# Kernel tuning notes

Measured on AMD Instinct MI355X. Metric: run time of the kernel, lower is better.

The kernel has to match this reference:

```python
import jax, jax.numpy as jnp
import numpy as np

LEAK = 0.01  # torch F.leaky_relu default
EPS = 1e-5   # torch LayerNorm default


def _ln(x, g, b):
    mu = jnp.mean(x, axis=-1, keepdims=True)
    var = jnp.var(x, axis=-1, keepdims=True)
    return (x - mu) * jax.lax.rsqrt(var + EPS) * g + b


def setup_inputs() -> dict:
    key = jax.random.key(0)
    ks = jax.random.split(key, 12)
    npeds, h, e = 8192, 256, 64
    s = 0.05
    return {
        "last_pos": jax.random.normal(ks[0], (npeds, 2), jnp.float32),
        "last_pos_rel": jax.random.normal(ks[1], (npeds, 2), jnp.float32),
        "h0": jax.random.normal(ks[2], (1, npeds, h), jnp.float32) * s,
        "c0": jax.random.normal(ks[3], (1, npeds, h), jnp.float32) * s,
        "W_ih": jax.random.normal(ks[4], (4 * h, e), jnp.float32) * s,
        "W_hh": jax.random.normal(ks[5], (4 * h, h), jnp.float32) * s,
        "b_ih": jax.random.normal(ks[6], (4 * h,), jnp.float32) * s,
        "b_hh": jax.random.normal(ks[7], (4 * h,), jnp.float32) * s,
        "emb_W": jax.random.normal(ks[8], (e, 2), jnp.float32) * s,
        "emb_b": jax.random.normal(ks[9], (e,), jnp.float32) * s,
        "ln1_g": jnp.ones((2,), jnp.float32),
        "ln1_b": jnp.zeros((2,), jnp.float32),
        "pos_W": jax.random.normal(ks[10], (2, h), jnp.float32) * s,
        "pos_b": jax.random.normal(ks[11], (2,), jnp.float32) * s,
        "ln2_g": jnp.ones((h,), jnp.float32),
        "ln2_b": jnp.zeros((h,), jnp.float32),
    }


def reference(last_pos, last_pos_rel, h0, c0, W_ih, W_hh, b_ih, b_hh,
              emb_W, emb_b, ln1_g, ln1_b, pos_W, pos_b, ln2_g, ln2_b):
    seq_len = 30
    h_dim = W_hh.shape[1]
    bias = b_ih + b_hh

    def embed(p):  # leaky_relu(spatial_embedding(ln1(p)))
        return jax.nn.leaky_relu(_ln(p, ln1_g, ln1_b) @ emb_W.T + emb_b, LEAK)

    def step(carry, _):
        dec_in, h, c, lp = carry  # dec_in [N,e], h/c [N,H], lp [N,2]
        gates = dec_in @ W_ih.T + h @ W_hh.T + bias  # [N,4H]
        i, f, g, o = jnp.split(gates, 4, axis=-1)    # torch gate order i,f,g,o
        c = jax.nn.sigmoid(f) * c + jax.nn.sigmoid(i) * jnp.tanh(g)
        h = jax.nn.sigmoid(o) * jnp.tanh(c)
        rel = jax.nn.sigmoid(_ln(h, ln2_g, ln2_b) @ pos_W.T + pos_b)  # [N,2]
        lp = rel + lp
        return (embed(rel), h, c, lp), rel

    carry0 = (embed(last_pos_rel), h0[0], c0[0], last_pos)
    _, rels = jax.lax.scan(step, carry0, None, length=seq_len)
    return rels  # [seq_len, npeds, 2]
```

## Files before the change

### kernel.cpp

```cpp
#include <hip/hip_runtime.h>


typedef float  f32x4  __attribute__((ext_vector_type(4)));
typedef short  short8 __attribute__((ext_vector_type(8)));
typedef __bf16 bf16x8 __attribute__((ext_vector_type(8)));
typedef int    i32x4  __attribute__((ext_vector_type(4)));

#define WS_W     0
#define WS_HBUF  (640 * 1024)
#define WS_BIAS  (WS_HBUF + 8388608)
#define WS_SCAL  (WS_BIAS + 4096)
#define WS_CTR   (WS_SCAL + 64)

__device__ __forceinline__ unsigned short f2bf(float f) {
  unsigned int u = __float_as_uint(f);
  u += 0x7FFFu + ((u >> 16) & 1u);
  return (unsigned short)(u >> 16);
}
__device__ __forceinline__ float bf2f(short s) {
  return __uint_as_float(((unsigned int)(unsigned short)s) << 16);
}
__device__ __forceinline__ float sigm(float x) {
  return __builtin_amdgcn_rcpf(1.0f + __expf(-x));
}
__device__ __forceinline__ float tanh_(float x) {
  float ax = fabsf(x);
  float t = __expf(-2.0f * ax);
  float r = (1.0f - t) * __builtin_amdgcn_rcpf(1.0f + t);
  return x >= 0.0f ? r : -r;
}
__device__ __forceinline__ f32x4 mfma16(short8 a, short8 b, f32x4 c) {
  return __builtin_amdgcn_mfma_f32_16x16x32_bf16(
      __builtin_bit_cast(bf16x8, a), __builtin_bit_cast(bf16x8, b), c, 0, 0, 0);
}
__device__ __forceinline__ void sc_store16(void* p, i32x4 v) {
  asm volatile("global_store_dwordx4 %0, %1, off sc0 sc1" ::"v"(p), "v"(v)
               : "memory");
}
__device__ __forceinline__ void drain_vm() {
  asm volatile("s_waitcnt vmcnt(0)" ::: "memory");
}
__device__ __forceinline__ void batch_load6(const i32x4* p0, const i32x4* p1,
                                            const i32x4* p2, const i32x4* p3,
                                            const i32x4* p4, const i32x4* p5,
                                            i32x4& r0, i32x4& r1, i32x4& r2,
                                            i32x4& r3, i32x4& r4, i32x4& r5) {
  asm volatile(
      "global_load_dwordx4 %0, %6, off sc0 sc1\n\t"
      "global_load_dwordx4 %1, %7, off sc0 sc1\n\t"
      "global_load_dwordx4 %2, %8, off sc0 sc1\n\t"
      "global_load_dwordx4 %3, %9, off sc0 sc1\n\t"
      "global_load_dwordx4 %4, %10, off sc0 sc1\n\t"
      "global_load_dwordx4 %5, %11, off sc0 sc1\n\t"
      "s_waitcnt vmcnt(0)"
      : "=&v"(r0), "=&v"(r1), "=&v"(r2), "=&v"(r3), "=&v"(r4), "=&v"(r5)
      : "v"(p0), "v"(p1), "v"(p2), "v"(p3), "v"(p4), "v"(p5)
      : "memory");
}

extern "C" __global__ void shuffle_weights(const float* __restrict__ Wih,
                                           const float* __restrict__ Whh,
                                           unsigned short* __restrict__ ws_w) {
  int t = blockIdx.x * 256 + threadIdx.x;
  if (t >= 40960) return;
  int l = t & 63;
  int x = t >> 6;
  int uw = x & 3;
  int g = (x >> 2) & 3;
  int y = x >> 4;
  int kc = y % 10;
  int ug = y / 10;
  int row = g * 256 + ug * 64 + uw * 16 + (l & 15);
  unsigned short* dst = ws_w + (size_t)t * 8;
  if (kc < 2) {
    const float* src = Wih + row * 64 + kc * 32 + (l >> 4) * 8;
#pragma unroll
    for (int j = 0; j < 8; j++) dst[j] = f2bf(src[j]);
  } else {
    const float* src = Whh + row * 256 + (kc - 2) * 32 + (l >> 4) * 8;
#pragma unroll
    for (int j = 0; j < 8; j++) dst[j] = f2bf(src[j]);
  }
}

extern "C" __global__ void prologue2(const float* __restrict__ b_ih,
                                     const float* __restrict__ b_hh,
                                     const float* __restrict__ ln2g,
                                     const float* __restrict__ ln2b,
                                     const float* __restrict__ posW,
                                     float* __restrict__ biasv,
                                     float* __restrict__ scal,
                                     int* __restrict__ ctr) {
  int t = threadIdx.x;
#pragma unroll
  for (int k2 = 0; k2 < 4; k2++) {
    int n = t * 4 + k2;
    biasv[n] = b_ih[n] + b_hh[n];
  }
  if (t < 64) ctr[t * 64] = 0;
  __shared__ float red[256][4];
  float g = ln2g[t], b = ln2b[t], p0 = posW[t], p1 = posW[256 + t];
  red[t][0] = b * p0;
  red[t][1] = b * p1;
  red[t][2] = g * p0;
  red[t][3] = g * p1;
  __syncthreads();
  for (int s = 128; s > 0; s >>= 1) {
    if (t < s) {
#pragma unroll
      for (int v = 0; v < 4; v++) red[t][v] += red[t + s][v];
    }
    __syncthreads();
  }
  if (t == 0) {
#pragma unroll
    for (int v = 0; v < 4; v++) scal[v] = red[0][v];
  }
}

extern "C" __global__ __launch_bounds__(512, 2) void decoder_main(
    const float* __restrict__ lpr, const float* __restrict__ h0,
    const float* __restrict__ c0, const float* __restrict__ embW,
    const float* __restrict__ embB, const float* __restrict__ ln1g,
    const float* __restrict__ ln1b, const float* __restrict__ posW,
    const float* __restrict__ posB, const float* __restrict__ ln2g,
    const unsigned short* __restrict__ ws_w,
    unsigned short* __restrict__ hbuf,
    const float* __restrict__ biasv, const float* __restrict__ scal,
    int* __restrict__ ctr, float* __restrict__ out) {
  __shared__ unsigned short w_lds[4 * 16 * 512];
  __shared__ unsigned short h_stage[8 * 8 * 512];
  __shared__ unsigned short xh[16 * 512];
  __shared__ float ppt[512];
  __shared__ float n01[128][2];

  const int bid = blockIdx.x;
  const int pg = bid >> 2, ug = bid & 3;
  const int tid = threadIdx.x;
  const int w = tid >> 6, l = tid & 63;
  const int uw = w & 3, pw = w >> 2;
  const int q = l >> 4, li = l & 15;
  const int P0 = pg * 128;
  const int loff = l * 8;
  const int u = ug * 64 + uw * 16 + li;

  {
    const unsigned short* src = ws_w + (size_t)ug * 81920;
#pragma unroll
    for (int it = 0; it < 8; it++) {
      int f = tid + it * 512;
      *(short8*)(w_lds + f * 8) = *(const short8*)(src + f * 8);
    }
  }
  short8 wr[6][4];
#pragma unroll
  for (int kk = 0; kk < 6; kk++)
#pragma unroll
    for (int g = 0; g < 4; g++)
      wr[kk][g] = *(const short8*)(ws_w + (size_t)ug * 81920 +
                                   ((kk + 4) * 16 + g * 4 + uw) * 512 + loff);

  const float K0 = scal[0], K1 = scal[1], SP0 = scal[2], SP1 = scal[3];
  const float pb0 = posB[0], pb1 = posB[1];
  const float g10 = ln1g[0], g11 = ln1g[1], b10 = ln1b[0], b11 = ln1b[1];

  float bias_r[4];
#pragma unroll
  for (int g = 0; g < 4; g++) bias_r[g] = biasv[g * 256 + u];

  {
    int uu = tid & 255, r = tid >> 8;
    ppt[uu * 2 + r] = ln2g[uu] * posW[r * 256 + uu];
  }

  f32x4 c_r[4];
#pragma unroll
  for (int mt = 0; mt < 4; mt++)
#pragma unroll
    for (int r = 0; r < 4; r++)
      c_r[mt][r] = c0[(size_t)(P0 + pw * 64 + mt * 16 + q * 4 + r) * 256 + u];

#pragma unroll
  for (int it = 0; it < 8; it++) {
    int f = tid + it * 512;
    int ll = f & 63, kc = (f >> 6) & 7, Tl = f >> 9;
    const float* src =
        h0 + (size_t)(P0 + Tl * 16 + (ll & 15)) * 256 + kc * 32 + (ll >> 4) * 8;
    float tf[8];
    *(float4*)&tf[0] = *(const float4*)(src);
    *(float4*)&tf[4] = *(const float4*)(src + 4);
    short8 sv;
#pragma unroll
    for (int j = 0; j < 8; j++) sv[j] = (short)f2bf(tf[j]);
    *(short8*)(h_stage + f * 8) = sv;
  }

  if (tid < 128) {
    float r0 = lpr[(P0 + tid) * 2], r1 = lpr[(P0 + tid) * 2 + 1];
    float d = 0.5f * (r0 - r1);
    float rs = rsqrtf(d * d + 1e-5f);
    n01[tid][0] = d * rs * g10 + b10;
    n01[tid][1] = -d * rs * g11 + b11;
  }
  __syncthreads();

  {
    const int pc = tid >> 2, s4 = tid & 3;
    float n0 = n01[pc][0], n1 = n01[pc][1];
    int Tl = pc >> 4, row = pc & 15;
#pragma unroll
    for (int jj = 0; jj < 16; jj++) {
      int k = s4 * 16 + jj;
      float e = n0 * embW[k * 2] + n1 * embW[k * 2 + 1] + embB[k];
      e = e > 0.f ? e : 0.01f * e;
      xh[(Tl * 2 + (k >> 5)) * 512 + (row + 16 * ((k & 31) >> 3)) * 8 + (k & 7)] =
          f2bf(e);
    }
  }
  __syncthreads();

  i32x4* hb4 = (i32x4*)hbuf;

  for (int st = 0; st < 30; st++) {
    const size_t pbase = (size_t)(st & 1) * 262144;

    f32x4 acc[4][4];
#pragma unroll
    for (int g = 0; g < 4; g++)
#pragma unroll
      for (int mt = 0; mt < 4; mt++)
        acc[g][mt] = (f32x4){bias_r[g], bias_r[g], bias_r[g], bias_r[g]};

#pragma unroll
    for (int kc2 = 0; kc2 < 2; kc2++) {
      short8 ax[4];
#pragma unroll
      for (int mt = 0; mt < 4; mt++)
        ax[mt] = *(const short8*)(xh + ((pw * 4 + mt) * 2 + kc2) * 512 + loff);
#pragma unroll
      for (int g = 0; g < 4; g++) {
        short8 b = *(const short8*)(w_lds + (kc2 * 16 + g * 4 + uw) * 512 + loff);
#pragma unroll
        for (int mt = 0; mt < 4; mt++)
          acc[g][mt] = mfma16(ax[mt], b, acc[g][mt]);
      }
    }
#pragma unroll
    for (int kc = 0; kc < 8; kc++) {
      short8 a[4];
#pragma unroll
      for (int mt = 0; mt < 4; mt++)
        a[mt] = *(const short8*)(h_stage + ((pw * 4 + mt) * 8 + kc) * 512 + loff);
      if (kc < 2) {
#pragma unroll
        for (int g = 0; g < 4; g++) {
          short8 b =
              *(const short8*)(w_lds + ((kc + 2) * 16 + g * 4 + uw) * 512 + loff);
#pragma unroll
          for (int mt = 0; mt < 4; mt++)
            acc[g][mt] = mfma16(a[mt], b, acc[g][mt]);
        }
      } else {
#pragma unroll
        for (int g = 0; g < 4; g++)
#pragma unroll
          for (int mt = 0; mt < 4; mt++)
            acc[g][mt] = mfma16(a[mt], wr[kc - 2][g], acc[g][mt]);
      }
    }
    __syncthreads();

#pragma unroll
    for (int mt = 0; mt < 4; mt++) {
#pragma unroll
      for (int r = 0; r < 4; r++) {
        float iv = sigm(acc[0][mt][r]);
        float fv = sigm(acc[1][mt][r]);
        float gv = tanh_(acc[2][mt][r]);
        float ov = sigm(acc[3][mt][r]);
        float cc = fv * c_r[mt][r] + iv * gv;
        c_r[mt][r] = cc;
        float hv = ov * tanh_(cc);
        xh[((pw * 4 + mt) * 2 + (uw >> 1)) * 512 +
           ((q * 4 + r) + 16 * ((uw & 1) * 2 + (li >> 3))) * 8 + (li & 7)] =
            f2bf(hv);
      }
    }
    __syncthreads();

    i32x4 vown[2];
    {
      const i32x4* xh4 = (const i32x4*)xh;
#pragma unroll
      for (int it = 0; it < 2; it++) {
        int f = tid + it * 512;
        int s = f & 63, c = f >> 6, Tl = c >> 1, kcl = c & 1;
        vown[it] = xh4[f];
        sc_store16(hb4 + pbase + (((size_t)(pg * 8 + Tl)) * 8 + 2 * ug + kcl) * 64 + s,
                   vown[it]);
      }
      drain_vm();
    }
    __syncthreads();

    if (tid == 0) {
      __hip_atomic_fetch_add(ctr + pg * 64, 1, __ATOMIC_RELAXED,
                             __HIP_MEMORY_SCOPE_AGENT);
      int target = 4 * (st + 1);
      while (__hip_atomic_load(ctr + pg * 64, __ATOMIC_RELAXED,
                               __HIP_MEMORY_SCOPE_AGENT) < target)
        __builtin_amdgcn_s_sleep(1);
    }
    __syncthreads();

    {
      const i32x4* ps[6];
      int Tls[6], kcs[6], ss[6];
#pragma unroll
      for (int it = 0; it < 6; it++) {
        int f = tid + it * 512;
        int s = f & 63, x = f >> 6;
        int Tl = x / 6, j = x - Tl * 6;
        int kc = j + (j >= 2 * ug ? 2 : 0);
        Tls[it] = Tl; kcs[it] = kc; ss[it] = s;
        ps[it] = hb4 + pbase + (((size_t)(pg * 8 + Tl)) * 8 + kc) * 64 + s;
      }
      i32x4 r0, r1, r2, r3, r4, r5;
      batch_load6(ps[0], ps[1], ps[2], ps[3], ps[4], ps[5], r0, r1, r2, r3, r4,
                  r5);
      i32x4* hs4 = (i32x4*)h_stage;
      hs4[(Tls[0] * 8 + kcs[0]) * 64 + ss[0]] = r0;
      hs4[(Tls[1] * 8 + kcs[1]) * 64 + ss[1]] = r1;
      hs4[(Tls[2] * 8 + kcs[2]) * 64 + ss[2]] = r2;
      hs4[(Tls[3] * 8 + kcs[3]) * 64 + ss[3]] = r3;
      hs4[(Tls[4] * 8 + kcs[4]) * 64 + ss[4]] = r4;
      hs4[(Tls[5] * 8 + kcs[5]) * 64 + ss[5]] = r5;
#pragma unroll
      for (int it = 0; it < 2; it++) {
        int f = tid + it * 512;
        int s = f & 63, c = f >> 6, Tl = c >> 1, kcl = c & 1;
        hs4[(Tl * 8 + 2 * ug + kcl) * 64 + s] = vown[it];
      }
    }
    __syncthreads();

    {
      const int pl = tid >> 2, part = tid & 3;
      const int Tl = pl >> 4, row = pl & 15;
      float S = 0.f, S2 = 0.f, D0 = 0.f, D1 = 0.f;
#pragma unroll
      for (int kk = 0; kk < 2; kk++) {
        int kcx = part * 2 + kk;
#pragma unroll
        for (int sub = 0; sub < 4; sub++) {
          short8 h8 = *(const short8*)(h_stage + (Tl * 8 + kcx) * 512 +
                                       (row + 16 * sub) * 8);
          const float4* pp = (const float4*)(ppt + (kcx * 32 + sub * 8) * 2);
#pragma unroll
          for (int k4 = 0; k4 < 4; k4++) {
            float4 pv = pp[k4];
            float ha = bf2f(h8[2 * k4]);
            float hb = bf2f(h8[2 * k4 + 1]);
            S += ha + hb;
            S2 += ha * ha + hb * hb;
            D0 += ha * pv.x + hb * pv.z;
            D1 += ha * pv.y + hb * pv.w;
          }
        }
      }
      S += __shfl_xor(S, 1, 64);  S += __shfl_xor(S, 2, 64);
      S2 += __shfl_xor(S2, 1, 64); S2 += __shfl_xor(S2, 2, 64);
      D0 += __shfl_xor(D0, 1, 64); D0 += __shfl_xor(D0, 2, 64);
      D1 += __shfl_xor(D1, 1, 64); D1 += __shfl_xor(D1, 2, 64);
      if (part == 0) {
        float mu = S * (1.0f / 256.0f);
        float var = S2 * (1.0f / 256.0f) - mu * mu;
        float rsig = rsqrtf(var + 1e-5f);
        float rel0 = sigm(rsig * (D0 - mu * SP0) + K0 + pb0);
        float rel1 = sigm(rsig * (D1 - mu * SP1) + K1 + pb1);
        if (ug == 0)
          *(float2*)(out + (size_t)st * 16384 + (P0 + pl) * 2) =
              make_float2(rel0, rel1);
        float d = 0.5f * (rel0 - rel1);
        float rs = rsqrtf(d * d + 1e-5f);
        n01[pl][0] = d * rs * g10 + b10;
        n01[pl][1] = -d * rs * g11 + b11;
      }
    }
    __syncthreads();

    if (st < 29) {
      const int pc = tid >> 2, s4 = tid & 3;
      float n0 = n01[pc][0], n1 = n01[pc][1];
      int Tl = pc >> 4, row = pc & 15;
#pragma unroll
      for (int jj = 0; jj < 16; jj++) {
        int k = s4 * 16 + jj;
        float e = n0 * embW[k * 2] + n1 * embW[k * 2 + 1] + embB[k];
        e = e > 0.f ? e : 0.01f * e;
        xh[(Tl * 2 + (k >> 5)) * 512 + (row + 16 * ((k & 31) >> 3)) * 8 +
           (k & 7)] = f2bf(e);
      }
    }
    __syncthreads();
  }
}

extern "C" void kernel_launch(void* const* d_in, const int* in_sizes, int n_in,
                              void* d_out, int out_size, void* d_ws,
                              size_t ws_size, hipStream_t stream) {
  (void)in_sizes; (void)n_in; (void)out_size; (void)ws_size;
  const float* lpr  = (const float*)d_in[1];
  const float* h0   = (const float*)d_in[2];
  const float* c0   = (const float*)d_in[3];
  const float* Wih  = (const float*)d_in[4];
  const float* Whh  = (const float*)d_in[5];
  const float* b_ih = (const float*)d_in[6];
  const float* b_hh = (const float*)d_in[7];
  const float* embW = (const float*)d_in[8];
  const float* embB = (const float*)d_in[9];
  const float* ln1g = (const float*)d_in[10];
  const float* ln1b = (const float*)d_in[11];
  const float* posW = (const float*)d_in[12];
  const float* posB = (const float*)d_in[13];
  const float* ln2g = (const float*)d_in[14];
  const float* ln2b = (const float*)d_in[15];

  char* ws = (char*)d_ws;
  unsigned short* ws_w = (unsigned short*)(ws + WS_W);
  unsigned short* hbuf = (unsigned short*)(ws + WS_HBUF);
  float* biasv  = (float*)(ws + WS_BIAS);
  float* scal   = (float*)(ws + WS_SCAL);
  int*   ctr    = (int*)(ws + WS_CTR);

  shuffle_weights<<<dim3(160), dim3(256), 0, stream>>>(Wih, Whh, ws_w);
  prologue2<<<dim3(1), dim3(256), 0, stream>>>(b_ih, b_hh, ln2g, ln2b, posW,
                                               biasv, scal, ctr);
  decoder_main<<<dim3(256), dim3(512), 0, stream>>>(
      lpr, h0, c0, embW, embB, ln1g, ln1b, posW, posB, ln2g, ws_w, hbuf,
      biasv, scal, ctr, (float*)d_out);
}
```

Before: 671.2 us.

## Compute LayerNorm/projection partial stats in registers and exchange via global buffer

```diff
diff --git a/kernel.cpp b/kernel.cpp
--- a/kernel.cpp
+++ b/kernel.cpp
@@ -8,7 +8,8 @@
 
 #define WS_W     0
 #define WS_HBUF  (640 * 1024)
-#define WS_BIAS  (WS_HBUF + 8388608)
+#define WS_SBUF  (WS_HBUF + 8388608)
+#define WS_BIAS  (WS_SBUF + 1048576)
 #define WS_SCAL  (WS_BIAS + 4096)
 #define WS_CTR   (WS_SCAL + 64)
 
@@ -16,9 +17,6 @@
   unsigned int u = __float_as_uint(f);
   u += 0x7FFFu + ((u >> 16) & 1u);
   return (unsigned short)(u >> 16);
-}
-__device__ __forceinline__ float bf2f(short s) {
-  return __uint_as_float(((unsigned int)(unsigned short)s) << 16);
 }
 __device__ __forceinline__ float sigm(float x) {
   return __builtin_amdgcn_rcpf(1.0f + __expf(-x));
@@ -40,21 +38,22 @@
 __device__ __forceinline__ void drain_vm() {
   asm volatile("s_waitcnt vmcnt(0)" ::: "memory");
 }
-__device__ __forceinline__ void batch_load6(const i32x4* p0, const i32x4* p1,
-                                            const i32x4* p2, const i32x4* p3,
-                                            const i32x4* p4, const i32x4* p5,
-                                            i32x4& r0, i32x4& r1, i32x4& r2,
-                                            i32x4& r3, i32x4& r4, i32x4& r5) {
+__device__ __forceinline__ void batch_load7(
+    const i32x4* p0, const i32x4* p1, const i32x4* p2, const i32x4* p3,
+    const i32x4* p4, const i32x4* p5, const i32x4* p6, i32x4& r0, i32x4& r1,
+    i32x4& r2, i32x4& r3, i32x4& r4, i32x4& r5, i32x4& r6) {
   asm volatile(
-      "global_load_dwordx4 %0, %6, off sc0 sc1\n\t"
-      "global_load_dwordx4 %1, %7, off sc0 sc1\n\t"
-      "global_load_dwordx4 %2, %8, off sc0 sc1\n\t"
-      "global_load_dwordx4 %3, %9, off sc0 sc1\n\t"
-      "global_load_dwordx4 %4, %10, off sc0 sc1\n\t"
-      "global_load_dwordx4 %5, %11, off sc0 sc1\n\t"
+      "global_load_dwordx4 %0, %7, off sc0 sc1\n\t"
+      "global_load_dwordx4 %1, %8, off sc0 sc1\n\t"
+      "global_load_dwordx4 %2, %9, off sc0 sc1\n\t"
+      "global_load_dwordx4 %3, %10, off sc0 sc1\n\t"
+      "global_load_dwordx4 %4, %11, off sc0 sc1\n\t"
+      "global_load_dwordx4 %5, %12, off sc0 sc1\n\t"
+      "global_load_dwordx4 %6, %13, off sc0 sc1\n\t"
       "s_waitcnt vmcnt(0)"
-      : "=&v"(r0), "=&v"(r1), "=&v"(r2), "=&v"(r3), "=&v"(r4), "=&v"(r5)
-      : "v"(p0), "v"(p1), "v"(p2), "v"(p3), "v"(p4), "v"(p5)
+      : "=&v"(r0), "=&v"(r1), "=&v"(r2), "=&v"(r3), "=&v"(r4), "=&v"(r5),
+        "=&v"(r6)
+      : "v"(p0), "v"(p1), "v"(p2), "v"(p3), "v"(p4), "v"(p5), "v"(p6)
       : "memory");
 }
 
@@ -126,12 +125,14 @@
     const float* __restrict__ posB, const float* __restrict__ ln2g,
     const unsigned short* __restrict__ ws_w,
     unsigned short* __restrict__ hbuf,
+    float* __restrict__ sbuf,
     const float* __restrict__ biasv, const float* __restrict__ scal,
     int* __restrict__ ctr, float* __restrict__ out) {
   __shared__ unsigned short w_lds[4 * 16 * 512];
   __shared__ unsigned short h_stage[8 * 8 * 512];
   __shared__ unsigned short xh[16 * 512];
-  __shared__ float ppt[512];
+  __shared__ float partials[128 * 16];
+  __shared__ float statl[384 * 4];
   __shared__ float n01[128][2];
 
   const int bid = blockIdx.x;
@@ -167,10 +168,11 @@
   float bias_r[4];
 #pragma unroll
   for (int g = 0; g < 4; g++) bias_r[g] = biasv[g * 256 + u];
-
+  float Pp0, Pp1;
   {
-    int uu = tid & 255, r = tid >> 8;
-    ppt[uu * 2 + r] = ln2g[uu] * posW[r * 256 + uu];
+    float gg = ln2g[u];
+    Pp0 = gg * posW[u];
+    Pp1 = gg * posW[256 + u];
   }
 
   f32x4 c_r[4];
@@ -220,9 +222,11 @@
   __syncthreads();
 
   i32x4* hb4 = (i32x4*)hbuf;
+  i32x4* sb4 = (i32x4*)sbuf;
 
   for (int st = 0; st < 30; st++) {
     const size_t pbase = (size_t)(st & 1) * 262144;
+    const size_t sbase = (size_t)(st & 1) * 32768;
 
     f32x4 acc[4][4];
 #pragma unroll
@@ -272,6 +276,7 @@
 
 #pragma unroll
     for (int mt = 0; mt < 4; mt++) {
+      float sh[4], sh2[4], sA[4], sB[4];
 #pragma unroll
       for (int r = 0; r < 4; r++) {
         float iv = sigm(acc[0][mt][r]);
@@ -284,20 +289,54 @@
         xh[((pw * 4 + mt) * 2 + (uw >> 1)) * 512 +
            ((q * 4 + r) + 16 * ((uw & 1) * 2 + (li >> 3))) * 8 + (li & 7)] =
             f2bf(hv);
-      }
-    }
-    __syncthreads();
-
-    i32x4 vown[2];
+        sh[r] = hv;
+        sh2[r] = hv * hv;
+        sA[r] = hv * Pp0;
+        sB[r] = hv * Pp1;
+      }
+#pragma unroll
+      for (int mask = 1; mask <= 8; mask <<= 1) {
+#pragma unroll
+        for (int r = 0; r < 4; r++) {
+          sh[r] += __shfl_xor(sh[r], mask, 64);
+          sh2[r] += __shfl_xor(sh2[r], mask, 64);
+          sA[r] += __shfl_xor(sA[r], mask, 64);
+          sB[r] += __shfl_xor(sB[r], mask, 64);
+        }
+      }
+      if (li == 0) {
+#pragma unroll
+        for (int r = 0; r < 4; r++)
+          *(f32x4*)(partials + (pw * 64 + mt * 16 + q * 4 + r) * 16 + uw * 4) =
+              (f32x4){sh[r], sh2[r], sA[r], sB[r]};
+      }
+    }
+    __syncthreads();
+
+    f32x4 sown = (f32x4){0.f, 0.f, 0.f, 0.f};
     {
       const i32x4* xh4 = (const i32x4*)xh;
+      i32x4* hs4 = (i32x4*)h_stage;
 #pragma unroll
       for (int it = 0; it < 2; it++) {
         int f = tid + it * 512;
         int s = f & 63, c = f >> 6, Tl = c >> 1, kcl = c & 1;
-        vown[it] = xh4[f];
-        sc_store16(hb4 + pbase + (((size_t)(pg * 8 + Tl)) * 8 + 2 * ug + kcl) * 64 + s,
-                   vown[it]);
+        i32x4 v = xh4[f];
+        hs4[(Tl * 8 + 2 * ug + kcl) * 64 + s] = v;
+        sc_store16(hb4 + pbase +
+                       (((size_t)(pg * 8 + Tl)) * 8 + 2 * ug + kcl) * 64 + s,
+                   v);
+      }
+      if (tid < 128) {
+        f32x4 sv = *(const f32x4*)(partials + tid * 16);
+#pragma unroll
+        for (int uu = 1; uu < 4; uu++) {
+          f32x4 t2 = *(const f32x4*)(partials + tid * 16 + uu * 4);
+          sv.x += t2.x; sv.y += t2.y; sv.z += t2.z; sv.w += t2.w;
+        }
+        sown = sv;
+        sc_store16(sb4 + sbase + ((size_t)pg * 4 + ug) * 128 + tid,
+                   __builtin_bit_cast(i32x4, sv));
       }
       drain_vm();
     }
@@ -314,7 +353,7 @@
     __syncthreads();
 
     {
-      const i32x4* ps[6];
+      const i32x4* ps[7];
       int Tls[6], kcs[6], ss[6];
 #pragma unroll
       for (int it = 0; it < 6; it++) {
@@ -325,9 +364,13 @@
         Tls[it] = Tl; kcs[it] = kc; ss[it] = s;
         ps[it] = hb4 + pbase + (((size_t)(pg * 8 + Tl)) * 8 + kc) * 64 + s;
       }
-      i32x4 r0, r1, r2, r3, r4, r5;
-      batch_load6(ps[0], ps[1], ps[2], ps[3], ps[4], ps[5], r0, r1, r2, r3, r4,
-                  r5);
+      int spi = tid >> 7, sped = tid & 127;
+      int pu = (spi < 3) ? (spi + (spi >= ug ? 1 : 0)) : ug;
+      ps[6] = sb4 + sbase + ((size_t)pg * 4 + pu) * 128 + sped;
+
+      i32x4 r0, r1, r2, r3, r4, r5, r6;
+      batch_load7(ps[0], ps[1], ps[2], ps[3], ps[4], ps[5], ps[6], r0, r1, r2,
+                  r3, r4, r5, r6);
       i32x4* hs4 = (i32x4*)h_stage;
       hs4[(Tls[0] * 8 + kcs[0]) * 64 + ss[0]] = r0;
       hs4[(Tls[1] * 8 + kcs[1]) * 64 + ss[1]] = r1;
@@ -335,57 +378,29 @@
       hs4[(Tls[3] * 8 + kcs[3]) * 64 + ss[3]] = r3;
       hs4[(Tls[4] * 8 + kcs[4]) * 64 + ss[4]] = r4;
       hs4[(Tls[5] * 8 + kcs[5]) * 64 + ss[5]] = r5;
-#pragma unroll
-      for (int it = 0; it < 2; it++) {
-        int f = tid + it * 512;
-        int s = f & 63, c = f >> 6, Tl = c >> 1, kcl = c & 1;
-        hs4[(Tl * 8 + 2 * ug + kcl) * 64 + s] = vown[it];
-      }
-    }
-    __syncthreads();
-
-    {
-      const int pl = tid >> 2, part = tid & 3;
-      const int Tl = pl >> 4, row = pl & 15;
-      float S = 0.f, S2 = 0.f, D0 = 0.f, D1 = 0.f;
-#pragma unroll
-      for (int kk = 0; kk < 2; kk++) {
-        int kcx = part * 2 + kk;
-#pragma unroll
-        for (int sub = 0; sub < 4; sub++) {
-          short8 h8 = *(const short8*)(h_stage + (Tl * 8 + kcx) * 512 +
-                                       (row + 16 * sub) * 8);
-          const float4* pp = (const float4*)(ppt + (kcx * 32 + sub * 8) * 2);
-#pragma unroll
-          for (int k4 = 0; k4 < 4; k4++) {
-            float4 pv = pp[k4];
-            float ha = bf2f(h8[2 * k4]);
-            float hb = bf2f(h8[2 * k4 + 1]);
-            S += ha + hb;
-            S2 += ha * ha + hb * hb;
-            D0 += ha * pv.x + hb * pv.z;
-            D1 += ha * pv.y + hb * pv.w;
-          }
-        }
-      }
-      S += __shfl_xor(S, 1, 64);  S += __shfl_xor(S, 2, 64);
-      S2 += __shfl_xor(S2, 1, 64); S2 += __shfl_xor(S2, 2, 64);
-      D0 += __shfl_xor(D0, 1, 64); D0 += __shfl_xor(D0, 2, 64);
-      D1 += __shfl_xor(D1, 1, 64); D1 += __shfl_xor(D1, 2, 64);
-      if (part == 0) {
-        float mu = S * (1.0f / 256.0f);
-        float var = S2 * (1.0f / 256.0f) - mu * mu;
-        float rsig = rsqrtf(var + 1e-5f);
-        float rel0 = sigm(rsig * (D0 - mu * SP0) + K0 + pb0);
-        float rel1 = sigm(rsig * (D1 - mu * SP1) + K1 + pb1);
-        if (ug == 0)
-          *(float2*)(out + (size_t)st * 16384 + (P0 + pl) * 2) =
-              make_float2(rel0, rel1);
-        float d = 0.5f * (rel0 - rel1);
-        float rs = rsqrtf(d * d + 1e-5f);
-        n01[pl][0] = d * rs * g10 + b10;
-        n01[pl][1] = -d * rs * g11 + b11;
-      }
+      if (tid < 384) *(i32x4*)(statl + tid * 4) = r6;
+    }
+    __syncthreads();
+
+    if (tid < 128) {
+      float S = sown.x, S2 = sown.y, D0 = sown.z, D1 = sown.w;
+#pragma unroll
+      for (int p = 0; p < 3; p++) {
+        f32x4 v = *(const f32x4*)(statl + (p * 128 + tid) * 4);
+        S += v.x; S2 += v.y; D0 += v.z; D1 += v.w;
+      }
+      float mu = S * (1.0f / 256.0f);
+      float var = S2 * (1.0f / 256.0f) - mu * mu;
+      float rsig = rsqrtf(var + 1e-5f);
+      float rel0 = sigm(rsig * (D0 - mu * SP0) + K0 + pb0);
+      float rel1 = sigm(rsig * (D1 - mu * SP1) + K1 + pb1);
+      if (ug == 0)
+        *(float2*)(out + (size_t)st * 16384 + (P0 + tid) * 2) =
+            make_float2(rel0, rel1);
+      float d = 0.5f * (rel0 - rel1);
+      float rs = rsqrtf(d * d + 1e-5f);
+      n01[tid][0] = d * rs * g10 + b10;
+      n01[tid][1] = -d * rs * g11 + b11;
     }
     __syncthreads();
 
@@ -429,6 +444,7 @@
   char* ws = (char*)d_ws;
   unsigned short* ws_w = (unsigned short*)(ws + WS_W);
   unsigned short* hbuf = (unsigned short*)(ws + WS_HBUF);
+  float* sbufp  = (float*)(ws + WS_SBUF);
   float* biasv  = (float*)(ws + WS_BIAS);
   float* scal   = (float*)(ws + WS_SCAL);
   int*   ctr    = (int*)(ws + WS_CTR);
@@ -438,5 +454,5 @@
                                                biasv, scal, ctr);
   decoder_main<<<dim3(256), dim3(512), 0, stream>>>(
       lpr, h0, c0, embW, embB, ln1g, ln1b, posW, posB, ln2g, ws_w, hbuf,
-      biasv, scal, ctr, (float*)d_out);
-}
+      sbufp, biasv, scal, ctr, (float*)d_out);
+}
```

Result: slower. 746.9 us (+11.3%).
